# Kernel optimization log

Measured on AMD Instinct MI355X. Metric: run time of the kernel, lower is better.

The kernel has to match this reference:

```python
import jax, jax.numpy as jnp
import numpy as np

B = 8          # batch (decode: one new token per sequence)
L = 2          # layers
DIM = 1024
H = 8
HD = DIM // H  # 128
BS = 16        # KV-cache block size
SEQ = 2048
TT = SEQ + 1                     # context after appending the new token
NB = (TT + BS - 1) // BS         # 129 logical blocks per sequence
HEAP = L * B * NB                # 2064 physical blocks in the heap
SCALE = 1.0 / float(np.sqrt(HD))
EPS = 1e-5
NEG = -1e30


def rmsnorm(x, w):
    return x * jax.lax.rsqrt(jnp.mean(x * x, axis=-1, keepdims=True) + EPS) * w


def setup_inputs() -> dict:
    key = jax.random.key(0)
    ks = jax.random.split(key, 12)
    s = 0.02
    x = jax.random.normal(ks[0], (B, DIM), jnp.float32)
    # paged KV heaps, layout [phys_block, block_offset, head, head_dim]
    key_heap = jax.random.normal(ks[1], (HEAP, BS, H, HD), jnp.float32)
    val_heap = jax.random.normal(ks[2], (HEAP, BS, H, HD), jnp.float32)
    # each (layer, batch) owns a disjoint contiguous block range
    block_tables = jnp.arange(L * B * NB, dtype=jnp.int32).reshape(L, B, NB)
    lb, off = SEQ // BS, SEQ % BS  # logical block / offset of the new token
    slot_mapping = block_tables[:, :, lb].astype(jnp.int64) * BS + off  # [L, B]
    context_lens = jnp.full((B,), TT, dtype=jnp.int32)
    wq = jax.random.normal(ks[3], (L, DIM, DIM), jnp.float32) * s
    wk = jax.random.normal(ks[4], (L, DIM, DIM), jnp.float32) * s
    wv = jax.random.normal(ks[5], (L, DIM, DIM), jnp.float32) * s
    wo = jax.random.normal(ks[6], (L, DIM, DIM), jnp.float32) * s
    w1 = jax.random.normal(ks[7], (L, 4 * DIM, DIM), jnp.float32) * s
    w2 = jax.random.normal(ks[8], (L, DIM, 4 * DIM), jnp.float32) * s
    w3 = jax.random.normal(ks[9], (L, 4 * DIM, DIM), jnp.float32) * s
    norm1_w = jnp.ones((L, DIM), jnp.float32)
    norm2_w = jnp.ones((L, DIM), jnp.float32)
    norm_w = jnp.ones((DIM,), jnp.float32)
    return {"x": x, "key_heap": key_heap, "val_heap": val_heap,
            "block_tables": block_tables, "slot_mapping": slot_mapping,
            "context_lens": context_lens, "wq": wq, "wk": wk, "wv": wv,
            "wo": wo, "w1": w1, "w2": w2, "w3": w3,
            "norm1_w": norm1_w, "norm2_w": norm2_w, "norm_w": norm_w}


def reference(x, key_heap, val_heap, block_tables, slot_mapping, context_lens,
              wq, wk, wv, wo, w1, w2, w3, norm1_w, norm2_w, norm_w):
    pos = jnp.arange(NB * BS, dtype=jnp.int32).reshape(NB, BS)  # logical token index
    for l in range(L):
        # --- attention sub-block ---
        residual = x
        h = rmsnorm(x, norm1_w[l])
        q = (h @ wq[l].T).reshape(B, H, HD)
        k = (h @ wk[l].T).reshape(B, H, HD)
        v = (h @ wv[l].T).reshape(B, H, HD)
        # reshape_and_cache: scatter the new token's K/V into the paged heap
        sm = slot_mapping[l]              # [B]
        blk, off = sm // BS, sm % BS
        key_heap = key_heap.at[blk, off].set(k)
        val_heap = val_heap.at[blk, off].set(v)
        # paged_attention_v2: gather blocks via block table, masked softmax
        bt = block_tables[l]              # [B, NB]
        Kb = key_heap[bt]                 # [B, NB, BS, H, HD]
        Vb = val_heap[bt]
        scores = jnp.einsum('bhd,bnshd->bhns', q, Kb) * SCALE  # [B, H, NB, BS]
        mask = (pos[None] < context_lens[:, None, None])[:, None]  # [B, 1, NB, BS]
        scores = jnp.where(mask, scores, NEG)
        p = jax.nn.softmax(scores.reshape(B, H, NB * BS), axis=-1).reshape(B, H, NB, BS)
        attn = jnp.einsum('bhns,bnshd->bhd', p, Vb).reshape(B, H * HD)
        x = attn @ wo[l].T + residual
        # --- SwiGLU FFN sub-block ---
        residual = x
        h = rmsnorm(x, norm2_w[l])
        x = (jax.nn.silu(h @ w1[l].T) * (h @ w3[l].T)) @ w2[l].T + residual
    return rmsnorm(x, norm_w)
```

## Files before the change

### kernel.cpp

```cpp
#include <hip/hip_runtime.h>

#define BB    8
#define LL    2
#define DIM   1024
#define NH    8
#define HD    128
#define BS    16
#define NB    129
#define NSPLIT 32
#define SCALE 0.08838834764831845f
#define EPS   1e-5f

__global__ void rmsnorm_k(const float* __restrict__ x, const float* __restrict__ w,
                          float* __restrict__ out) {
  int b = blockIdx.x;
  float4 v = ((const float4*)(x + (size_t)b * DIM))[threadIdx.x];
  float s = v.x * v.x + v.y * v.y + v.z * v.z + v.w * v.w;
#pragma unroll
  for (int o = 32; o; o >>= 1) s += __shfl_xor(s, o);
  __shared__ float wsum[4];
  int wid = threadIdx.x >> 6;
  if ((threadIdx.x & 63) == 0) wsum[wid] = s;
  __syncthreads();
  float tot = wsum[0] + wsum[1] + wsum[2] + wsum[3];
  float r = rsqrtf(tot * (1.0f / DIM) + EPS);
  float4 wv = ((const float4*)w)[threadIdx.x];
  float4 o;
  o.x = v.x * r * wv.x; o.y = v.y * r * wv.y;
  o.z = v.z * r * wv.z; o.w = v.w * r * wv.w;
  ((float4*)(out + (size_t)b * DIM))[threadIdx.x] = o;
}

__device__ __forceinline__ void block_rms_scales(const float ss[8], float* lds,
                                                 float* scale) {
  int tid = threadIdx.x;
#pragma unroll
  for (int b = 0; b < 8; ++b) lds[tid * 9 + b] = ss[b];
  __syncthreads();
  int bb = tid >> 5, i = tid & 31;
  float s = 0.0f;
#pragma unroll
  for (int j = 0; j < 8; ++j) s += lds[(i + 32 * j) * 9 + bb];
#pragma unroll
  for (int o = 16; o; o >>= 1) s += __shfl_xor(s, o);
  if (i == 0) scale[bb] = rsqrtf(s * (1.0f / DIM) + EPS);
  __syncthreads();
}

__device__ __forceinline__ float block_reduce8(const float acc[8], float* lds,
                                               int* bb_out) {
  int tid = threadIdx.x;
#pragma unroll
  for (int b = 0; b < 8; ++b) lds[tid * 9 + b] = acc[b];
  __syncthreads();
  int bb = tid >> 5, i = tid & 31;
  float s = 0.0f;
#pragma unroll
  for (int j = 0; j < 8; ++j) s += lds[(i + 32 * j) * 9 + bb];
#pragma unroll
  for (int o = 16; o; o >>= 1) s += __shfl_xor(s, o);
  *bb_out = bb;
  return s;
}

__global__ void qkv_k(const float* __restrict__ x, const float* __restrict__ nw,
                      const float* __restrict__ wq, const float* __restrict__ wk,
                      const float* __restrict__ wv,
                      float* __restrict__ q, float* __restrict__ k, float* __restrict__ v) {
  __shared__ float lds[256 * 9];
  __shared__ float scale[8];
  int tid = threadIdx.x;
  float4 xr[8];
  float ss[8];
#pragma unroll
  for (int bb = 0; bb < 8; ++bb) {
    xr[bb] = *(const float4*)(x + bb * DIM + tid * 4);
    ss[bb] = xr[bb].x * xr[bb].x + xr[bb].y * xr[bb].y +
             xr[bb].z * xr[bb].z + xr[bb].w * xr[bb].w;
  }
  block_rms_scales(ss, lds, scale);

  int row = blockIdx.x;
  int mat = row >> 10, r = row & 1023;
  const float* W = (mat == 0 ? wq : mat == 1 ? wk : wv) + (size_t)r * DIM;
  float4 wn = *(const float4*)(nw + tid * 4);
  float4 w4 = *(const float4*)(W + tid * 4);
  float acc[8];
#pragma unroll
  for (int bb = 0; bb < 8; ++bb) {
    acc[bb] = w4.x * (xr[bb].x * wn.x) + w4.y * (xr[bb].y * wn.y) +
              w4.z * (xr[bb].z * wn.z) + w4.w * (xr[bb].w * wn.w);
  }
  int bb; float s = block_reduce8(acc, lds, &bb);
  if ((tid & 31) == 0) {
    float* dst = (mat == 0 ? q : mat == 1 ? k : v);
    dst[bb * DIM + r] = s * scale[bb];
  }
}

__global__ void proj_res_k(const float* __restrict__ in, const float* __restrict__ W0,
                           const float* __restrict__ resid, float* __restrict__ out) {
  __shared__ float lds[256 * 9];
  int r = blockIdx.x;
  int tid = threadIdx.x;
  float4 w4 = *(const float4*)(W0 + (size_t)r * DIM + tid * 4);
  float acc[8];
#pragma unroll
  for (int bb = 0; bb < 8; ++bb) {
    float4 h4 = *(const float4*)(in + bb * DIM + tid * 4);
    acc[bb] = w4.x * h4.x + w4.y * h4.y + w4.z * h4.z + w4.w * h4.w;
  }
  int bb; float s = block_reduce8(acc, lds, &bb);
  if ((tid & 31) == 0) out[bb * DIM + r] = s + resid[bb * DIM + r];
}

__global__ void ffn13_k(const float* __restrict__ xa, const float* __restrict__ nw,
                        const float* __restrict__ w1, const float* __restrict__ w3,
                        float* __restrict__ g) {
  __shared__ float ldsA[256 * 9];
  __shared__ float ldsC[256 * 9];
  __shared__ float scale[8];
  int tid = threadIdx.x;
  float4 xr[8];
  float ss[8];
#pragma unroll
  for (int bb = 0; bb < 8; ++bb) {
    xr[bb] = *(const float4*)(xa + bb * DIM + tid * 4);
    ss[bb] = xr[bb].x * xr[bb].x + xr[bb].y * xr[bb].y +
             xr[bb].z * xr[bb].z + xr[bb].w * xr[bb].w;
  }
  block_rms_scales(ss, ldsA, scale);

  int r = blockIdx.x;
  float4 wn = *(const float4*)(nw + tid * 4);
  float4 w14 = *(const float4*)(w1 + (size_t)r * DIM + tid * 4);
  float4 w34 = *(const float4*)(w3 + (size_t)r * DIM + tid * 4);
  float a[8], c[8];
#pragma unroll
  for (int bb = 0; bb < 8; ++bb) {
    float hx = xr[bb].x * wn.x, hy = xr[bb].y * wn.y;
    float hz = xr[bb].z * wn.z, hw = xr[bb].w * wn.w;
    a[bb] = w14.x * hx + w14.y * hy + w14.z * hz + w14.w * hw;
    c[bb] = w34.x * hx + w34.y * hy + w34.z * hz + w34.w * hw;
  }
#pragma unroll
  for (int b = 0; b < 8; ++b) { ldsA[tid * 9 + b] = a[b]; ldsC[tid * 9 + b] = c[b]; }
  __syncthreads();
  int bb = tid >> 5, i = tid & 31;
  float sa = 0.0f, sc = 0.0f;
#pragma unroll
  for (int j = 0; j < 8; ++j) {
    sa += ldsA[(i + 32 * j) * 9 + bb];
    sc += ldsC[(i + 32 * j) * 9 + bb];
  }
#pragma unroll
  for (int o = 16; o; o >>= 1) { sa += __shfl_xor(sa, o); sc += __shfl_xor(sc, o); }
  if (i == 0) {
    float sv = (sa * scale[bb]);
    sv = sv / (1.0f + __expf(-sv));
    g[bb * 4 * DIM + r] = sv * (sc * scale[bb]);
  }
}

__global__ void ffn2_k(const float* __restrict__ g, const float* __restrict__ w2,
                       const float* __restrict__ resid, float* __restrict__ out) {
  __shared__ float lds[256 * 9];
  int r = blockIdx.x;
  int tid = threadIdx.x;
  const float* W = w2 + (size_t)r * 4 * DIM;
  float acc[8] = {};
#pragma unroll
  for (int j4 = 0; j4 < 4; ++j4) {
    int j = j4 * 1024 + tid * 4;
    float4 w4 = *(const float4*)(W + j);
#pragma unroll
    for (int bb = 0; bb < 8; ++bb) {
      float4 g4 = *(const float4*)(g + bb * 4 * DIM + j);
      acc[bb] += w4.x * g4.x + w4.y * g4.y + w4.z * g4.z + w4.w * g4.w;
    }
  }
  int bb; float s = block_reduce8(acc, lds, &bb);
  if ((tid & 31) == 0) out[bb * DIM + r] = s + resid[bb * DIM + r];
}

__global__ void attn_partial_k(const float* __restrict__ qb, const float* __restrict__ kb,
                               const float* __restrict__ vb,
                               const float* __restrict__ kheap, const float* __restrict__ vheap,
                               const int* __restrict__ bt, const int* __restrict__ ctx_lens,
                               float* __restrict__ pm, float* __restrict__ ps,
                               float* __restrict__ pacc) {
  int c  = blockIdx.x;
  int bh = blockIdx.y;
  int b = bh >> 3, hh = bh & 7;
  int grp = threadIdx.x >> 5, lane = threadIdx.x & 31;
  int ctx = ctx_lens[b];
  int CH = (ctx + NSPLIT - 1) / NSPLIT;
  int t0 = c * CH;
  int t1 = t0 + CH; if (t1 > ctx) t1 = ctx;
  int last = ctx - 1;
  const float4 q4 = *(const float4*)(qb + (size_t)b * DIM + hh * HD + lane * 4);
  const int* btb = bt + b * NB;
  float m = -1e30f, ssum = 0.0f;
  float4 acc = make_float4(0.f, 0.f, 0.f, 0.f);
  for (int t = t0 + grp; t < t1; t += 8) {
    const float *Kp, *Vp;
    if (t == last) {
      Kp = kb + (size_t)b * DIM + hh * HD;
      Vp = vb + (size_t)b * DIM + hh * HD;
    } else {
      int pb = btb[t >> 4];
      size_t base = ((((size_t)pb * BS) + (t & 15)) * NH + hh) * HD;
      Kp = kheap + base;
      Vp = vheap + base;
    }
    float4 k4 = *(const float4*)(Kp + lane * 4);
    float sc = q4.x * k4.x + q4.y * k4.y + q4.z * k4.z + q4.w * k4.w;
#pragma unroll
    for (int o = 16; o; o >>= 1) sc += __shfl_xor(sc, o);
    sc *= SCALE;
    float mnew = fmaxf(m, sc);
    float f = __expf(m - mnew);
    float p = __expf(sc - mnew);
    float4 v4 = *(const float4*)(Vp + lane * 4);
    ssum = ssum * f + p;
    acc.x = acc.x * f + p * v4.x;
    acc.y = acc.y * f + p * v4.y;
    acc.z = acc.z * f + p * v4.z;
    acc.w = acc.w * f + p * v4.w;
    m = mnew;
  }
  int pi = bh * (NSPLIT * 8) + c * 8 + grp;
  if (lane == 0) { pm[pi] = m; ps[pi] = ssum; }
  *(float4*)(pacc + (size_t)pi * HD + lane * 4) = acc;
}

__global__ void attn_reduce_k(const float* __restrict__ pm, const float* __restrict__ ps,
                              const float* __restrict__ pacc, float* __restrict__ ab) {
  int bh = blockIdx.x;
  int tid = threadIdx.x;
  __shared__ float f[256];
  __shared__ float red[128];
  float m1 = pm[bh * 256 + tid];
  float m2 = pm[bh * 256 + 128 + tid];
  red[tid] = fmaxf(m1, m2); __syncthreads();
#pragma unroll
  for (int o = 64; o; o >>= 1) {
    if (tid < o) red[tid] = fmaxf(red[tid], red[tid + o]);
    __syncthreads();
  }
  float M = red[0];
  __syncthreads();
  float f1 = __expf(m1 - M), f2 = __expf(m2 - M);
  f[tid] = f1; f[tid + 128] = f2;
  red[tid] = ps[bh * 256 + tid] * f1 + ps[bh * 256 + 128 + tid] * f2;
  __syncthreads();
#pragma unroll
  for (int o = 64; o; o >>= 1) {
    if (tid < o) red[tid] += red[tid + o];
    __syncthreads();
  }
  float inv = 1.0f / red[0];
  float od = 0.0f;
  for (int p = 0; p < 256; ++p)
    od += pacc[((size_t)bh * 256 + p) * HD + tid] * f[p];
  ab[bh * HD + tid] = od * inv;
}

extern "C" void kernel_launch(void* const* d_in, const int* in_sizes, int n_in,
                              void* d_out, int out_size, void* d_ws, size_t ws_size,
                              hipStream_t stream) {
  const float* x0    = (const float*)d_in[0];
  const float* kheap = (const float*)d_in[1];
  const float* vheap = (const float*)d_in[2];
  const int*   bt    = (const int*)d_in[3];
  const int*   ctx   = (const int*)d_in[5];
  const float* wq    = (const float*)d_in[6];
  const float* wk    = (const float*)d_in[7];
  const float* wv    = (const float*)d_in[8];
  const float* wo    = (const float*)d_in[9];
  const float* w1    = (const float*)d_in[10];
  const float* w2    = (const float*)d_in[11];
  const float* w3    = (const float*)d_in[12];
  const float* norm1 = (const float*)d_in[13];
  const float* norm2 = (const float*)d_in[14];
  const float* normf = (const float*)d_in[15];

  float* ws = (float*)d_ws;
  float* q    = ws;
  float* k    = ws + 8192;
  float* v    = ws + 16384;
  float* g    = ws + 24576;
  float* xa   = ws + 57344;
  float* xf   = ws + 65536;
  float* ab   = ws + 73728;
  float* pm   = ws + 81920;
  float* ps   = ws + 98304;
  float* pacc = ws + 114688;

  const size_t WD = (size_t)DIM * DIM;
  const size_t WF = (size_t)4 * DIM * DIM;

  for (int l = 0; l < LL; ++l) {
    const float* xin = (l == 0) ? x0 : xf;
    qkv_k<<<3072, 256, 0, stream>>>(xin, norm1 + l * DIM,
                                    wq + l * WD, wk + l * WD, wv + l * WD, q, k, v);
    attn_partial_k<<<dim3(NSPLIT, BB * NH), 256, 0, stream>>>(
        q, k, v, kheap, vheap, bt + l * BB * NB, ctx, pm, ps, pacc);
    attn_reduce_k<<<BB * NH, 128, 0, stream>>>(pm, ps, pacc, ab);
    proj_res_k<<<1024, 256, 0, stream>>>(ab, wo + l * WD, xin, xa);
    ffn13_k<<<4096, 256, 0, stream>>>(xa, norm2 + l * DIM, w1 + l * WF, w3 + l * WF, g);
    ffn2_k<<<1024, 256, 0, stream>>>(g, w2 + l * WF, xa, xf);
  }
  rmsnorm_k<<<BB, 256, 0, stream>>>(xf, normf, (float*)d_out);
}
```

Baseline: 155.1 us.

## Fuse attention reduce and final rmsnorm into producers via last-block atomic counters

The separate attention-reduce kernel is folded into attn_partial_k: each split block increments a per-(batch,head) counter, and the last block to arrive merges the partial softmax states. In the same way, the final rmsnorm is folded into the last layer's ffn2_k through a global done counter. The V load is also hoisted ahead of the score reduction so its latency overlaps. This removes two kernel launches per forward pass at the cost of a memset, threadfences, atomics, and a tail phase that runs serially in a single block.

```diff
diff --git a/kernel.cpp b/kernel.cpp
--- a/kernel.cpp
+++ b/kernel.cpp
@@ -11,24 +11,10 @@
 #define SCALE 0.08838834764831845f
 #define EPS   1e-5f
 
-__global__ void rmsnorm_k(const float* __restrict__ x, const float* __restrict__ w,
-                          float* __restrict__ out) {
-  int b = blockIdx.x;
-  float4 v = ((const float4*)(x + (size_t)b * DIM))[threadIdx.x];
-  float s = v.x * v.x + v.y * v.y + v.z * v.z + v.w * v.w;
-#pragma unroll
-  for (int o = 32; o; o >>= 1) s += __shfl_xor(s, o);
-  __shared__ float wsum[4];
-  int wid = threadIdx.x >> 6;
-  if ((threadIdx.x & 63) == 0) wsum[wid] = s;
-  __syncthreads();
-  float tot = wsum[0] + wsum[1] + wsum[2] + wsum[3];
-  float r = rsqrtf(tot * (1.0f / DIM) + EPS);
-  float4 wv = ((const float4*)w)[threadIdx.x];
-  float4 o;
-  o.x = v.x * r * wv.x; o.y = v.y * r * wv.y;
-  o.z = v.z * r * wv.z; o.w = v.w * r * wv.w;
-  ((float4*)(out + (size_t)b * DIM))[threadIdx.x] = o;
+__device__ __forceinline__ float wave_reduce_add(float v) {
+#pragma unroll
+  for (int o = 32; o; o >>= 1) v += __shfl_xor(v, o);
+  return v;
 }
 
 __device__ __forceinline__ void block_rms_scales(const float ss[8], float* lds,
@@ -59,6 +45,7 @@
   for (int j = 0; j < 8; ++j) s += lds[(i + 32 * j) * 9 + bb];
 #pragma unroll
   for (int o = 16; o; o >>= 1) s += __shfl_xor(s, o);
+  __syncthreads();
   *bb_out = bb;
   return s;
 }
@@ -98,101 +85,18 @@
   }
 }
 
-__global__ void proj_res_k(const float* __restrict__ in, const float* __restrict__ W0,
-                           const float* __restrict__ resid, float* __restrict__ out) {
-  __shared__ float lds[256 * 9];
-  int r = blockIdx.x;
-  int tid = threadIdx.x;
-  float4 w4 = *(const float4*)(W0 + (size_t)r * DIM + tid * 4);
-  float acc[8];
-#pragma unroll
-  for (int bb = 0; bb < 8; ++bb) {
-    float4 h4 = *(const float4*)(in + bb * DIM + tid * 4);
-    acc[bb] = w4.x * h4.x + w4.y * h4.y + w4.z * h4.z + w4.w * h4.w;
-  }
-  int bb; float s = block_reduce8(acc, lds, &bb);
-  if ((tid & 31) == 0) out[bb * DIM + r] = s + resid[bb * DIM + r];
-}
-
-__global__ void ffn13_k(const float* __restrict__ xa, const float* __restrict__ nw,
-                        const float* __restrict__ w1, const float* __restrict__ w3,
-                        float* __restrict__ g) {
-  __shared__ float ldsA[256 * 9];
-  __shared__ float ldsC[256 * 9];
-  __shared__ float scale[8];
-  int tid = threadIdx.x;
-  float4 xr[8];
-  float ss[8];
-#pragma unroll
-  for (int bb = 0; bb < 8; ++bb) {
-    xr[bb] = *(const float4*)(xa + bb * DIM + tid * 4);
-    ss[bb] = xr[bb].x * xr[bb].x + xr[bb].y * xr[bb].y +
-             xr[bb].z * xr[bb].z + xr[bb].w * xr[bb].w;
-  }
-  block_rms_scales(ss, ldsA, scale);
-
-  int r = blockIdx.x;
-  float4 wn = *(const float4*)(nw + tid * 4);
-  float4 w14 = *(const float4*)(w1 + (size_t)r * DIM + tid * 4);
-  float4 w34 = *(const float4*)(w3 + (size_t)r * DIM + tid * 4);
-  float a[8], c[8];
-#pragma unroll
-  for (int bb = 0; bb < 8; ++bb) {
-    float hx = xr[bb].x * wn.x, hy = xr[bb].y * wn.y;
-    float hz = xr[bb].z * wn.z, hw = xr[bb].w * wn.w;
-    a[bb] = w14.x * hx + w14.y * hy + w14.z * hz + w14.w * hw;
-    c[bb] = w34.x * hx + w34.y * hy + w34.z * hz + w34.w * hw;
-  }
-#pragma unroll
-  for (int b = 0; b < 8; ++b) { ldsA[tid * 9 + b] = a[b]; ldsC[tid * 9 + b] = c[b]; }
-  __syncthreads();
-  int bb = tid >> 5, i = tid & 31;
-  float sa = 0.0f, sc = 0.0f;
-#pragma unroll
-  for (int j = 0; j < 8; ++j) {
-    sa += ldsA[(i + 32 * j) * 9 + bb];
-    sc += ldsC[(i + 32 * j) * 9 + bb];
-  }
-#pragma unroll
-  for (int o = 16; o; o >>= 1) { sa += __shfl_xor(sa, o); sc += __shfl_xor(sc, o); }
-  if (i == 0) {
-    float sv = (sa * scale[bb]);
-    sv = sv / (1.0f + __expf(-sv));
-    g[bb * 4 * DIM + r] = sv * (sc * scale[bb]);
-  }
-}
-
-__global__ void ffn2_k(const float* __restrict__ g, const float* __restrict__ w2,
-                       const float* __restrict__ resid, float* __restrict__ out) {
-  __shared__ float lds[256 * 9];
-  int r = blockIdx.x;
-  int tid = threadIdx.x;
-  const float* W = w2 + (size_t)r * 4 * DIM;
-  float acc[8] = {};
-#pragma unroll
-  for (int j4 = 0; j4 < 4; ++j4) {
-    int j = j4 * 1024 + tid * 4;
-    float4 w4 = *(const float4*)(W + j);
-#pragma unroll
-    for (int bb = 0; bb < 8; ++bb) {
-      float4 g4 = *(const float4*)(g + bb * 4 * DIM + j);
-      acc[bb] += w4.x * g4.x + w4.y * g4.y + w4.z * g4.z + w4.w * g4.w;
-    }
-  }
-  int bb; float s = block_reduce8(acc, lds, &bb);
-  if ((tid & 31) == 0) out[bb * DIM + r] = s + resid[bb * DIM + r];
-}
-
 __global__ void attn_partial_k(const float* __restrict__ qb, const float* __restrict__ kb,
                                const float* __restrict__ vb,
                                const float* __restrict__ kheap, const float* __restrict__ vheap,
                                const int* __restrict__ bt, const int* __restrict__ ctx_lens,
                                float* __restrict__ pm, float* __restrict__ ps,
-                               float* __restrict__ pacc) {
+                               float* __restrict__ pacc, float* __restrict__ ab,
+                               unsigned* __restrict__ done) {
   int c  = blockIdx.x;
   int bh = blockIdx.y;
   int b = bh >> 3, hh = bh & 7;
-  int grp = threadIdx.x >> 5, lane = threadIdx.x & 31;
+  int tid = threadIdx.x;
+  int grp = tid >> 5, lane = tid & 31;
   int ctx = ctx_lens[b];
   int CH = (ctx + NSPLIT - 1) / NSPLIT;
   int t0 = c * CH;
@@ -214,6 +118,7 @@
       Vp = vheap + base;
     }
     float4 k4 = *(const float4*)(Kp + lane * 4);
+    float4 v4 = *(const float4*)(Vp + lane * 4);
     float sc = q4.x * k4.x + q4.y * k4.y + q4.z * k4.z + q4.w * k4.w;
 #pragma unroll
     for (int o = 16; o; o >>= 1) sc += __shfl_xor(sc, o);
@@ -221,7 +126,6 @@
     float mnew = fmaxf(m, sc);
     float f = __expf(m - mnew);
     float p = __expf(sc - mnew);
-    float4 v4 = *(const float4*)(Vp + lane * 4);
     ssum = ssum * f + p;
     acc.x = acc.x * f + p * v4.x;
     acc.y = acc.y * f + p * v4.y;
@@ -229,41 +133,167 @@
     acc.w = acc.w * f + p * v4.w;
     m = mnew;
   }
-  int pi = bh * (NSPLIT * 8) + c * 8 + grp;
+  int pi = bh * 256 + c * 8 + grp;
   if (lane == 0) { pm[pi] = m; ps[pi] = ssum; }
   *(float4*)(pacc + (size_t)pi * HD + lane * 4) = acc;
-}
-
-__global__ void attn_reduce_k(const float* __restrict__ pm, const float* __restrict__ ps,
-                              const float* __restrict__ pacc, float* __restrict__ ab) {
-  int bh = blockIdx.x;
-  int tid = threadIdx.x;
-  __shared__ float f[256];
-  __shared__ float red[128];
-  float m1 = pm[bh * 256 + tid];
-  float m2 = pm[bh * 256 + 128 + tid];
-  red[tid] = fmaxf(m1, m2); __syncthreads();
-#pragma unroll
-  for (int o = 64; o; o >>= 1) {
-    if (tid < o) red[tid] = fmaxf(red[tid], red[tid + o]);
-    __syncthreads();
-  }
-  float M = red[0];
-  __syncthreads();
-  float f1 = __expf(m1 - M), f2 = __expf(m2 - M);
-  f[tid] = f1; f[tid + 128] = f2;
-  red[tid] = ps[bh * 256 + tid] * f1 + ps[bh * 256 + 128 + tid] * f2;
-  __syncthreads();
-#pragma unroll
-  for (int o = 64; o; o >>= 1) {
-    if (tid < o) red[tid] += red[tid + o];
-    __syncthreads();
-  }
-  float inv = 1.0f / red[0];
-  float od = 0.0f;
-  for (int p = 0; p < 256; ++p)
-    od += pacc[((size_t)bh * 256 + p) * HD + tid] * f[p];
-  ab[bh * HD + tid] = od * inv;
+
+  __shared__ int lastflag;
+  __shared__ float red[256];
+  __shared__ float fb[256];
+  __syncthreads();
+  if (tid == 0) {
+    __threadfence();
+    unsigned old = atomicAdd(&done[bh], 1u);
+    lastflag = (old == NSPLIT - 1);
+  }
+  __syncthreads();
+  if (lastflag) {
+    if (tid == 0) __threadfence();
+    __syncthreads();
+    float mi = pm[bh * 256 + tid];
+    red[tid] = mi; __syncthreads();
+#pragma unroll
+    for (int o = 128; o; o >>= 1) {
+      if (tid < o) red[tid] = fmaxf(red[tid], red[tid + o]);
+      __syncthreads();
+    }
+    float M = red[0]; __syncthreads();
+    float fi = __expf(mi - M);
+    fb[tid] = fi;
+    red[tid] = ps[bh * 256 + tid] * fi;
+    __syncthreads();
+#pragma unroll
+    for (int o = 128; o; o >>= 1) {
+      if (tid < o) red[tid] += red[tid + o];
+      __syncthreads();
+    }
+    float inv = 1.0f / red[0];
+    int d = tid & 127, hp = tid >> 7;
+    float od = 0.0f;
+    const float* pb2 = pacc + ((size_t)bh * 256 + hp * 128) * HD + d;
+    for (int p = 0; p < 128; ++p) od += pb2[(size_t)p * HD] * fb[hp * 128 + p];
+    __syncthreads();
+    red[tid] = od; __syncthreads();
+    if (tid < 128) ab[bh * HD + tid] = (red[tid] + red[tid + 128]) * inv;
+  }
+}
+
+__global__ void proj_res_k(const float* __restrict__ in, const float* __restrict__ W0,
+                           const float* __restrict__ resid, float* __restrict__ out) {
+  __shared__ float lds[256 * 9];
+  int r = blockIdx.x;
+  int tid = threadIdx.x;
+  float4 w4 = *(const float4*)(W0 + (size_t)r * DIM + tid * 4);
+  float acc[8];
+#pragma unroll
+  for (int bb = 0; bb < 8; ++bb) {
+    float4 h4 = *(const float4*)(in + bb * DIM + tid * 4);
+    acc[bb] = w4.x * h4.x + w4.y * h4.y + w4.z * h4.z + w4.w * h4.w;
+  }
+  int bb; float s = block_reduce8(acc, lds, &bb);
+  if ((tid & 31) == 0) out[bb * DIM + r] = s + resid[bb * DIM + r];
+}
+
+__global__ void ffn13_k(const float* __restrict__ xa, const float* __restrict__ nw,
+                        const float* __restrict__ w1, const float* __restrict__ w3,
+                        float* __restrict__ g) {
+  __shared__ float ldsA[256 * 9];
+  __shared__ float ldsC[256 * 9];
+  __shared__ float scale[8];
+  int tid = threadIdx.x;
+  float4 xr[8];
+  float ss[8];
+#pragma unroll
+  for (int bb = 0; bb < 8; ++bb) {
+    xr[bb] = *(const float4*)(xa + bb * DIM + tid * 4);
+    ss[bb] = xr[bb].x * xr[bb].x + xr[bb].y * xr[bb].y +
+             xr[bb].z * xr[bb].z + xr[bb].w * xr[bb].w;
+  }
+  block_rms_scales(ss, ldsA, scale);
+
+  int r = blockIdx.x;
+  float4 wn = *(const float4*)(nw + tid * 4);
+  float4 w14 = *(const float4*)(w1 + (size_t)r * DIM + tid * 4);
+  float4 w34 = *(const float4*)(w3 + (size_t)r * DIM + tid * 4);
+  float a[8], c[8];
+#pragma unroll
+  for (int bb = 0; bb < 8; ++bb) {
+    float hx = xr[bb].x * wn.x, hy = xr[bb].y * wn.y;
+    float hz = xr[bb].z * wn.z, hw = xr[bb].w * wn.w;
+    a[bb] = w14.x * hx + w14.y * hy + w14.z * hz + w14.w * hw;
+    c[bb] = w34.x * hx + w34.y * hy + w34.z * hz + w34.w * hw;
+  }
+#pragma unroll
+  for (int b = 0; b < 8; ++b) { ldsA[tid * 9 + b] = a[b]; ldsC[tid * 9 + b] = c[b]; }
+  __syncthreads();
+  int bb = tid >> 5, i = tid & 31;
+  float sa = 0.0f, sc = 0.0f;
+#pragma unroll
+  for (int j = 0; j < 8; ++j) {
+    sa += ldsA[(i + 32 * j) * 9 + bb];
+    sc += ldsC[(i + 32 * j) * 9 + bb];
+  }
+#pragma unroll
+  for (int o = 16; o; o >>= 1) { sa += __shfl_xor(sa, o); sc += __shfl_xor(sc, o); }
+  if (i == 0) {
+    float sv = sa * scale[bb];
+    sv = sv / (1.0f + __expf(-sv));
+    g[bb * 4 * DIM + r] = sv * (sc * scale[bb]);
+  }
+}
+
+__global__ void ffn2_k(const float* __restrict__ g, const float* __restrict__ w2,
+                       const float* __restrict__ resid, float* __restrict__ out,
+                       const float* __restrict__ normf, float* __restrict__ fout,
+                       unsigned* __restrict__ done2, int dofinal) {
+  __shared__ float lds[256 * 9];
+  int r = blockIdx.x;
+  int tid = threadIdx.x;
+  const float* W = w2 + (size_t)r * 4 * DIM;
+  float acc[8] = {};
+#pragma unroll
+  for (int j4 = 0; j4 < 4; ++j4) {
+    int j = j4 * 1024 + tid * 4;
+    float4 w4 = *(const float4*)(W + j);
+#pragma unroll
+    for (int bb = 0; bb < 8; ++bb) {
+      float4 g4 = *(const float4*)(g + bb * 4 * DIM + j);
+      acc[bb] += w4.x * g4.x + w4.y * g4.y + w4.z * g4.z + w4.w * g4.w;
+    }
+  }
+  int bb; float s = block_reduce8(acc, lds, &bb);
+  if ((tid & 31) == 0) out[bb * DIM + r] = s + resid[bb * DIM + r];
+
+  if (dofinal) {
+    __shared__ int lastf;
+    __shared__ float wsum[4];
+    __syncthreads();
+    if (tid == 0) {
+      __threadfence();
+      unsigned old = atomicAdd(done2, 1u);
+      lastf = (old == DIM - 1);
+    }
+    __syncthreads();
+    if (lastf) {
+      if (tid == 0) __threadfence();
+      __syncthreads();
+      for (int b = 0; b < BB; ++b) {
+        float4 vv = ((const float4*)(out + (size_t)b * DIM))[tid];
+        float ssq = vv.x * vv.x + vv.y * vv.y + vv.z * vv.z + vv.w * vv.w;
+        ssq = wave_reduce_add(ssq);
+        if ((tid & 63) == 0) wsum[tid >> 6] = ssq;
+        __syncthreads();
+        float tot = wsum[0] + wsum[1] + wsum[2] + wsum[3];
+        float rr = rsqrtf(tot * (1.0f / DIM) + EPS);
+        float4 wn = ((const float4*)normf)[tid];
+        float4 o4;
+        o4.x = vv.x * rr * wn.x; o4.y = vv.y * rr * wn.y;
+        o4.z = vv.z * rr * wn.z; o4.w = vv.w * rr * wn.w;
+        ((float4*)(fout + (size_t)b * DIM))[tid] = o4;
+        __syncthreads();
+      }
+    }
+  }
 }
 
 extern "C" void kernel_launch(void* const* d_in, const int* in_sizes, int n_in,
@@ -286,30 +316,33 @@
   const float* normf = (const float*)d_in[15];
 
   float* ws = (float*)d_ws;
-  float* q    = ws;
-  float* k    = ws + 8192;
-  float* v    = ws + 16384;
-  float* g    = ws + 24576;
-  float* xa   = ws + 57344;
-  float* xf   = ws + 65536;
-  float* ab   = ws + 73728;
-  float* pm   = ws + 81920;
-  float* ps   = ws + 98304;
-  float* pacc = ws + 114688;
+  unsigned* done  = (unsigned*)d_ws;
+  unsigned* done2 = done + 128;
+  float* q    = ws + 256;
+  float* k    = ws + 8448;
+  float* v    = ws + 16640;
+  float* g    = ws + 24832;
+  float* xa   = ws + 57600;
+  float* xf   = ws + 65792;
+  float* ab   = ws + 73984;
+  float* pm   = ws + 82176;
+  float* ps   = ws + 98560;
+  float* pacc = ws + 114944;
 
   const size_t WD = (size_t)DIM * DIM;
   const size_t WF = (size_t)4 * DIM * DIM;
+
+  hipMemsetAsync(d_ws, 0, 1024, stream);
 
   for (int l = 0; l < LL; ++l) {
     const float* xin = (l == 0) ? x0 : xf;
     qkv_k<<<3072, 256, 0, stream>>>(xin, norm1 + l * DIM,
                                     wq + l * WD, wk + l * WD, wv + l * WD, q, k, v);
     attn_partial_k<<<dim3(NSPLIT, BB * NH), 256, 0, stream>>>(
-        q, k, v, kheap, vheap, bt + l * BB * NB, ctx, pm, ps, pacc);
-    attn_reduce_k<<<BB * NH, 128, 0, stream>>>(pm, ps, pacc, ab);
+        q, k, v, kheap, vheap, bt + l * BB * NB, ctx, pm, ps, pacc, ab, done + l * 64);
     proj_res_k<<<1024, 256, 0, stream>>>(ab, wo + l * WD, xin, xa);
     ffn13_k<<<4096, 256, 0, stream>>>(xa, norm2 + l * DIM, w1 + l * WF, w3 + l * WF, g);
-    ffn2_k<<<1024, 256, 0, stream>>>(g, w2 + l * WF, xa, xf);
-  }
-  rmsnorm_k<<<BB, 256, 0, stream>>>(xf, normf, (float*)d_out);
-}
+    ffn2_k<<<1024, 256, 0, stream>>>(g, w2 + l * WF, xa, xf,
+                                     normf, (float*)d_out, done2, (l == LL - 1) ? 1 : 0);
+  }
+}
```

Measured after the change: 379.3 us. 145% more time.
